# Kernel optimization log

Measured on AMD Instinct MI355X. Metric: run time of the kernel, lower is better.

## Reference

```python
import jax, jax.numpy as jnp
import numpy as np

D_MODEL, D_INNER, D_STATE, DT_RANK, USERS = 2560, 5120, 16, 160, 32

def setup_inputs() -> dict:
    key = jax.random.key(0)
    ks = jax.random.split(key, 16)
    s = lambda k, shp, sc=0.02: (jax.random.normal(k, shp, dtype=jnp.float32) * sc)
    return {
        "x": jax.random.normal(ks[0], (1, 1, USERS, D_MODEL), dtype=jnp.float32),
        "w_in_ssm": s(ks[1], (D_MODEL, D_INNER)),
        "w_in_mlp": s(ks[2], (D_MODEL, D_INNER)),
        "w_out": s(ks[3], (D_INNER, D_MODEL)),
        "conv_w": s(ks[4], (4, D_INNER), 0.5),
        "conv_b": s(ks[5], (D_INNER,), 0.1),
        "conv_state1": jax.random.normal(ks[6], (1, 1, USERS, D_INNER), dtype=jnp.float32),
        "conv_state2": jax.random.normal(ks[7], (1, 1, USERS, D_INNER), dtype=jnp.float32),
        "conv_state3": jax.random.normal(ks[8], (1, 1, USERS, D_INNER), dtype=jnp.float32),
        "x_proj_w": s(ks[9], (D_INNER, DT_RANK + 2 * D_STATE)),
        "dt_proj_w": s(ks[10], (DT_RANK, D_INNER)),
        "dt_proj_b": s(ks[11], (D_INNER,), 0.1),
        "A_log": jax.random.uniform(ks[12], (D_INNER, D_STATE), dtype=jnp.float32),
        "D_param": s(ks[13], (D_INNER,), 1.0),
        "ssm_state": jax.random.normal(ks[14], (USERS, D_INNER, D_STATE), dtype=jnp.float32) * 0.1,
    }

def reference(x, w_in_ssm, w_in_mlp, w_out, conv_w, conv_b,
              conv_state1, conv_state2, conv_state3,
              x_proj_w, dt_proj_w, dt_proj_b, A_log, D_param, ssm_state):
    xb = x.reshape(USERS, D_MODEL)                       # [U, d_model]
    xs = xb @ w_in_ssm                                    # [U, d_inner] (newest conv tap)
    # 4-tap depthwise causal conv via shifted state buffer (unrolled in original)
    taps = (conv_state1.reshape(USERS, D_INNER),
            conv_state2.reshape(USERS, D_INNER),
            conv_state3.reshape(USERS, D_INNER),
            xs)
    c = taps[0] * conv_w[0] + taps[1] * conv_w[1] + taps[2] * conv_w[2] + taps[3] * conv_w[3] + conv_b
    c = jax.nn.silu(c)                                    # [U, d_inner]
    # selective SSM single-step update
    x_dbl = c @ x_proj_w                                  # [U, dt_rank + 2*d_state]
    dt = jax.nn.softplus(x_dbl[:, :DT_RANK] @ dt_proj_w + dt_proj_b)   # [U, d_inner]
    B = x_dbl[:, DT_RANK:DT_RANK + D_STATE]               # [U, d_state]
    C = x_dbl[:, DT_RANK + D_STATE:]                      # [U, d_state]
    A = -jnp.exp(A_log)                                   # [d_inner, d_state]
    dA = jnp.exp(dt[:, :, None] * A[None])                # [U, d_inner, d_state]
    new_state = ssm_state * dA + (dt * c)[:, :, None] * B[:, None, :]
    y = jnp.einsum("uds,us->ud", new_state, C) + D_param * c           # [U, d_inner]
    res = xb @ w_in_mlp                                   # gate branch (no extra silu, per source)
    out = (y * res) @ w_out                               # [U, d_model]
    return out.reshape(1, 1, USERS, D_MODEL)
```

## Files before the change

kernel.cpp:

```cpp
#include <hip/hip_runtime.h>
#include <hip/hip_bf16.h>
#include <cstdint>
#include <cstddef>

#define U   32
#define DM  2560
#define DI  5120
#define DS  16
#define RNK 160
#define XD  192
#define KC1 20
#define KC4 80

typedef __attribute__((ext_vector_type(8)))  short bf16x8;
typedef __attribute__((ext_vector_type(16))) float f32x16;

__device__ __forceinline__ unsigned int pkbf(float a, float b) {
  __hip_bfloat162 h = __float22bfloat162_rn(make_float2(a, b));
  union { __hip_bfloat162 h; unsigned int u; } v; v.h = h; return v.u;
}
__device__ __forceinline__ unsigned short f2bfu(float f) {
  __hip_bfloat16 h = __float2bfloat16(f);
  union { __hip_bfloat16 h; unsigned short u; } v; v.h = h; return v.u;
}
__device__ __forceinline__ float bf2f(unsigned int s) {
  union { float f; unsigned int u; } v; v.u = s << 16; return v.f;
}

__device__ __forceinline__ void gl_lds16(const float* g, float* l) {
  __builtin_amdgcn_global_load_lds(
      (const __attribute__((address_space(1))) unsigned int*)g,
      (__attribute__((address_space(3))) unsigned int*)l,
      16, 0, 0);
}

template<int LDW, int SLAB>
__global__ __launch_bounds__(256, 3) void skinny_dma(
    const float* __restrict__ A, int lda,
    const float* __restrict__ W0, const float* __restrict__ W1,
    unsigned short* __restrict__ part)
{
  constexpr int NS = SLAB / 16;
  __shared__ float        wbuf[2][16][256];
  __shared__ unsigned int albuf[NS][64][4];

  const int tid  = threadIdx.x;
  const int lane = tid & 63, w = tid >> 6;
  const int kcb  = blockIdx.y, z = blockIdx.z;
  const int k0   = kcb * SLAB;
  const float* __restrict__ W = z ? W1 : W0;
  const int col0 = blockIdx.x * 256;

  for (int i = tid; i < U * (SLAB / 2); i += 256) {
    const int u  = i / (SLAB / 2);
    const int kp = i - u * (SLAB / 2);
    const int k  = 2 * kp;
    const float2 v = *(const float2*)&A[(size_t)u * lda + k0 + k];
    albuf[k >> 4][u + U * ((k >> 3) & 1)][(k >> 1) & 3] = pkbf(v.x, v.y);
  }
  __syncthreads();

  const int cl = lane & 31, half = lane >> 5;

  const float* wsrc = W + ((size_t)k0 + w * 4) * LDW + col0 + lane * 4;

#pragma unroll
  for (int i = 0; i < 4; ++i)
    gl_lds16(wsrc + (size_t)i * LDW, &wbuf[0][w * 4 + i][0]);
#pragma unroll
  for (int i = 0; i < 4; ++i)
    gl_lds16(wsrc + (size_t)(16 + i) * LDW, &wbuf[1][w * 4 + i][0]);

  f32x16 acc0{}, acc1{};

#pragma unroll 1
  for (int s = 0; s < NS; ++s) {
    const int buf = s & 1;
    if (s + 1 < NS) { asm volatile("s_waitcnt vmcnt(4)" ::: "memory"); }
    else            { asm volatile("s_waitcnt vmcnt(0)" ::: "memory"); }
    __builtin_amdgcn_s_barrier();

    bf16x8 af = *(const bf16x8*)&albuf[s][lane][0];
#pragma unroll
    for (int f = 0; f < 2; ++f) {
      const int col = w * 64 + f * 32 + cl;
      float r0 = wbuf[buf][half * 8 + 0][col];
      float r1 = wbuf[buf][half * 8 + 1][col];
      float r2 = wbuf[buf][half * 8 + 2][col];
      float r3 = wbuf[buf][half * 8 + 3][col];
      float r4 = wbuf[buf][half * 8 + 4][col];
      float r5 = wbuf[buf][half * 8 + 5][col];
      float r6 = wbuf[buf][half * 8 + 6][col];
      float r7 = wbuf[buf][half * 8 + 7][col];
      union { bf16x8 v; unsigned int d[4]; } bu;
      bu.d[0] = pkbf(r0, r1); bu.d[1] = pkbf(r2, r3);
      bu.d[2] = pkbf(r4, r5); bu.d[3] = pkbf(r6, r7);
      if (f == 0) acc0 = __builtin_amdgcn_mfma_f32_32x32x16_bf16(af, bu.v, acc0, 0, 0, 0);
      else        acc1 = __builtin_amdgcn_mfma_f32_32x32x16_bf16(af, bu.v, acc1, 0, 0, 0);
    }

    asm volatile("" ::: "memory");
    __builtin_amdgcn_s_barrier();
    asm volatile("" ::: "memory");

    if (s + 2 < NS) {
      const float* src = wsrc + (size_t)(s + 2) * 16 * LDW;
#pragma unroll
      for (int i = 0; i < 4; ++i)
        gl_lds16(src + (size_t)i * LDW, &wbuf[buf][w * 4 + i][0]);
    }
  }

  unsigned short* po = part + (size_t)(z * gridDim.y + kcb) * U * LDW + col0;
#pragma unroll
  for (int f = 0; f < 2; ++f) {
    const f32x16& a = f ? acc1 : acc0;
    const int gc = w * 64 + f * 32 + cl;
#pragma unroll
    for (int r = 0; r < 16; ++r) {
      const int m = (r & 3) + 8 * (r >> 2) + 4 * half;
      po[(size_t)m * LDW + gc] = f2bfu(a[r]);
    }
  }
}

__global__ __launch_bounds__(256) void k2a_convsilu(
    const unsigned short* __restrict__ part,
    const float* __restrict__ cs1, const float* __restrict__ cs2,
    const float* __restrict__ cs3,
    const float* __restrict__ cw,  const float* __restrict__ cb,
    float* __restrict__ c_ws, float* __restrict__ res_ws)
{
  const int t = blockIdx.x * 256 + threadIdx.x;
  const int i = 2 * t;
  const int u = i / DI, d = i - u * DI;
  float xs0 = 0.f, xs1 = 0.f, rs0 = 0.f, rs1 = 0.f;
#pragma unroll 4
  for (int kc = 0; kc < KC1; ++kc) {
    unsigned int a = *(const unsigned int*)&part[((size_t)kc * U + u) * DI + d];
    unsigned int b = *(const unsigned int*)&part[((size_t)(KC1 + kc) * U + u) * DI + d];
    xs0 += bf2f(a & 0xffffu); xs1 += bf2f(a >> 16);
    rs0 += bf2f(b & 0xffffu); rs1 += bf2f(b >> 16);
  }
  const float2 s1 = *(const float2*)&cs1[i];
  const float2 s2 = *(const float2*)&cs2[i];
  const float2 s3 = *(const float2*)&cs3[i];
  const float2 w0 = *(const float2*)&cw[d];
  const float2 w1 = *(const float2*)&cw[DI + d];
  const float2 w2 = *(const float2*)&cw[2 * DI + d];
  const float2 w3 = *(const float2*)&cw[3 * DI + d];
  const float2 bb = *(const float2*)&cb[d];
  float c0 = s1.x * w0.x + s2.x * w1.x + s3.x * w2.x + xs0 * w3.x + bb.x;
  float c1 = s1.y * w0.y + s2.y * w1.y + s3.y * w2.y + xs1 * w3.y + bb.y;
  c0 = c0 / (1.f + __expf(-c0));
  c1 = c1 / (1.f + __expf(-c1));
  *(float2*)&c_ws[i]   = make_float2(c0, c1);
  *(float2*)&res_ws[i] = make_float2(rs0, rs1);
}

__global__ __launch_bounds__(256) void k2b_xproj(
    const float* __restrict__ c_ws,
    const float* __restrict__ xpw,
    float* __restrict__ x_dbl)
{
  __shared__ union { float ct[U][80]; float red[4][64][33]; } sh;
  const int k0 = blockIdx.y * 80;

  for (int i4 = threadIdx.x; i4 < U * 20; i4 += 256) {
    int u = i4 / 20, k4 = i4 - u * 20;
    *(float4*)&sh.ct[u][k4 * 4] = *(const float4*)&c_ws[u * DI + k0 + k4 * 4];
  }
  __syncthreads();

  const int c = threadIdx.x & 63, s = threadIdx.x >> 6;
  const int col = blockIdx.x * 64 + c;
  const float* Wp = xpw + (size_t)(k0 + s * 20) * XD + col;

  float acc[U];
#pragma unroll
  for (int u = 0; u < U; ++u) acc[u] = 0.f;

  for (int kk = 0; kk < 20; kk += 4) {
    float w0 = Wp[(size_t)(kk + 0) * XD];
    float w1 = Wp[(size_t)(kk + 1) * XD];
    float w2 = Wp[(size_t)(kk + 2) * XD];
    float w3 = Wp[(size_t)(kk + 3) * XD];
#pragma unroll
    for (int u = 0; u < U; ++u) {
      float4 cv = *(const float4*)&sh.ct[u][s * 20 + kk];
      acc[u] = fmaf(cv.x, w0, acc[u]);
      acc[u] = fmaf(cv.y, w1, acc[u]);
      acc[u] = fmaf(cv.z, w2, acc[u]);
      acc[u] = fmaf(cv.w, w3, acc[u]);
    }
  }

  __syncthreads();
#pragma unroll
  for (int u = 0; u < U; ++u) sh.red[s][c][u] = acc[u];
  __syncthreads();

  for (int p = threadIdx.x; p < 64 * U; p += 256) {
    int cc = p & 63, u = p >> 6;
    float v = sh.red[0][cc][u] + sh.red[1][cc][u] + sh.red[2][cc][u] + sh.red[3][cc][u];
    atomicAdd(&x_dbl[u * XD + blockIdx.x * 64 + cc], v);
  }
}

__global__ __launch_bounds__(256) void k3a_dt(
    const float* __restrict__ x_dbl,
    const float* __restrict__ dpw, const float* __restrict__ dpb,
    float* __restrict__ dt_ws)
{
  __shared__ union { float xt[U][160]; float red[4][64][33]; } sh;

  for (int i4 = threadIdx.x; i4 < U * 40; i4 += 256) {
    int u = i4 / 40, r4 = i4 - u * 40;
    *(float4*)&sh.xt[u][r4 * 4] = *(const float4*)&x_dbl[u * XD + r4 * 4];
  }
  __syncthreads();

  const int c = threadIdx.x & 63, s = threadIdx.x >> 6;
  const int d = blockIdx.x * 64 + c;
  const float* Wp = dpw + (size_t)(s * 40) * DI + d;

  float acc[U];
#pragma unroll
  for (int u = 0; u < U; ++u) acc[u] = 0.f;

  for (int rr = 0; rr < 40; rr += 4) {
    float w0 = Wp[(size_t)(rr + 0) * DI];
    float w1 = Wp[(size_t)(rr + 1) * DI];
    float w2 = Wp[(size_t)(rr + 2) * DI];
    float w3 = Wp[(size_t)(rr + 3) * DI];
#pragma unroll
    for (int u = 0; u < U; ++u) {
      float4 xv = *(const float4*)&sh.xt[u][s * 40 + rr];
      acc[u] = fmaf(xv.x, w0, acc[u]);
      acc[u] = fmaf(xv.y, w1, acc[u]);
      acc[u] = fmaf(xv.z, w2, acc[u]);
      acc[u] = fmaf(xv.w, w3, acc[u]);
    }
  }

  __syncthreads();
#pragma unroll
  for (int u = 0; u < U; ++u) sh.red[s][c][u] = acc[u];
  __syncthreads();

  for (int p = threadIdx.x; p < 64 * U; p += 256) {
    int cc = p & 63, u = p >> 6;
    int dg = blockIdx.x * 64 + cc;
    float pre = sh.red[0][cc][u] + sh.red[1][cc][u] + sh.red[2][cc][u] + sh.red[3][cc][u]
              + dpb[dg];
    float dt = fmaxf(pre, 0.f) + log1pf(expf(-fabsf(pre)));
    dt_ws[u * DI + dg] = dt;
  }
}

__global__ __launch_bounds__(256) void k3b_ssm(
    const float* __restrict__ x_dbl,
    const float* __restrict__ alog, const float* __restrict__ Dp,
    const float* __restrict__ ssm,
    const float* __restrict__ dt_ws,
    const float* __restrict__ c_ws, const float* __restrict__ res_ws,
    float* __restrict__ yr)
{
  const int i = blockIdx.x * 256 + threadIdx.x;
  const int u = i / DI, d = i - u * DI;

  const float dt = dt_ws[i];
  const float cv = c_ws[i];
  const float rv = res_ws[i];
  const float Dv = Dp[d];
  const float dtc = dt * cv;

  float4 B[4], C[4];
#pragma unroll
  for (int q = 0; q < 4; ++q) {
    B[q] = *(const float4*)&x_dbl[u * XD + RNK + q * 4];
    C[q] = *(const float4*)&x_dbl[u * XD + RNK + DS + q * 4];
  }

  const float* st = ssm + ((size_t)u * DI + d) * DS;
  float y = 0.f;
#pragma unroll
  for (int q = 0; q < 4; ++q) {
    float4 al = *(const float4*)&alog[d * DS + q * 4];
    float4 sv = *(const float4*)&st[q * 4];
    y += (sv.x * __expf(dt * -__expf(al.x)) + dtc * B[q].x) * C[q].x;
    y += (sv.y * __expf(dt * -__expf(al.y)) + dtc * B[q].y) * C[q].y;
    y += (sv.z * __expf(dt * -__expf(al.z)) + dtc * B[q].z) * C[q].z;
    y += (sv.w * __expf(dt * -__expf(al.w)) + dtc * B[q].w) * C[q].w;
  }
  y = fmaf(Dv, cv, y);
  yr[i] = y * rv;
}

__global__ __launch_bounds__(256) void k5_reduce(
    const unsigned short* __restrict__ part4,
    float* __restrict__ out)
{
  const int t = blockIdx.x * 256 + threadIdx.x;
  const int i = 2 * t;
  const int u = i / DM, d = i - u * DM;
  float v0 = 0.f, v1 = 0.f;
#pragma unroll 8
  for (int kc = 0; kc < KC4; ++kc) {
    unsigned int a = *(const unsigned int*)&part4[((size_t)kc * U + u) * DM + d];
    v0 += bf2f(a & 0xffffu);
    v1 += bf2f(a >> 16);
  }
  *(float2*)&out[i] = make_float2(v0, v1);
}

extern "C" void kernel_launch(void* const* d_in, const int* in_sizes, int n_in,
                              void* d_out, int out_size, void* d_ws, size_t ws_size,
                              hipStream_t stream)
{
  const float* x    = (const float*)d_in[0];
  const float* wssm = (const float*)d_in[1];
  const float* wmlp = (const float*)d_in[2];
  const float* wout = (const float*)d_in[3];
  const float* cw   = (const float*)d_in[4];
  const float* cb   = (const float*)d_in[5];
  const float* cs1  = (const float*)d_in[6];
  const float* cs2  = (const float*)d_in[7];
  const float* cs3  = (const float*)d_in[8];
  const float* xpw  = (const float*)d_in[9];
  const float* dpw  = (const float*)d_in[10];
  const float* dpb  = (const float*)d_in[11];
  const float* alog = (const float*)d_in[12];
  const float* Dp   = (const float*)d_in[13];
  const float* ssm  = (const float*)d_in[14];
  float* out = (float*)d_out;

  unsigned short* partb = (unsigned short*)d_ws;
  float* c_ws   = (float*)(partb + (size_t)2 * KC1 * U * DI);
  float* res_ws = c_ws   + (size_t)U * DI;
  float* dt_ws  = res_ws + (size_t)U * DI;
  float* yrb    = dt_ws  + (size_t)U * DI;
  float* x_dbl  = yrb    + (size_t)U * DI;

  (void)hipMemsetAsync(x_dbl, 0, (size_t)U * XD * sizeof(float), stream);

  skinny_dma<DI, 128><<<dim3(20, KC1, 2), 256, 0, stream>>>(x, DM, wssm, wmlp, partb);
  k2a_convsilu<<<320, 256, 0, stream>>>(partb, cs1, cs2, cs3, cw, cb, c_ws, res_ws);
  k2b_xproj<<<dim3(3, 64), 256, 0, stream>>>(c_ws, xpw, x_dbl);
  k3a_dt<<<80, 256, 0, stream>>>(x_dbl, dpw, dpb, dt_ws);
  k3b_ssm<<<640, 256, 0, stream>>>(x_dbl, alog, Dp, ssm, dt_ws, c_ws, res_ws, yrb);
  skinny_dma<DM, 64><<<dim3(10, KC4, 1), 256, 0, stream>>>(yrb, DI, wout, wout, partb);
  k5_reduce<<<160, 256, 0, stream>>>(partb, out);
}
```

Before: 86.57 us.

## Fuse middle stages into one cooperative kernel with grid syncs

Merges the conv/silu, x_proj, dt_proj and SSM-update kernels, plus the x_dbl memset, into a single cooperative kernel of 640 blocks that separates the stages with grid.sync(). The aim is to remove several kernel launches and the gaps between them on a latency-bound decode step. In exchange, grid-wide barriers have their own cost, shared memory becomes a union sized to the largest stage, and many blocks sit idle during the narrow x_proj and dt stages. If the cooperative launch fails, it falls back to separate kernels.

```diff
diff --git a/kernel.cpp b/kernel.cpp
--- a/kernel.cpp
+++ b/kernel.cpp
@@ -1,7 +1,10 @@
 #include <hip/hip_runtime.h>
 #include <hip/hip_bf16.h>
+#include <hip/hip_cooperative_groups.h>
 #include <cstdint>
 #include <cstddef>
+
+namespace cg = cooperative_groups;
 
 #define U   32
 #define DM  2560
@@ -61,7 +64,6 @@
   __syncthreads();
 
   const int cl = lane & 31, half = lane >> 5;
-
   const float* wsrc = W + ((size_t)k0 + w * 4) * LDW + col0 + lane * 4;
 
 #pragma unroll
@@ -124,14 +126,14 @@
   }
 }
 
-__global__ __launch_bounds__(256) void k2a_convsilu(
+__device__ __forceinline__ void k2a_body(
+    int t,
     const unsigned short* __restrict__ part,
     const float* __restrict__ cs1, const float* __restrict__ cs2,
     const float* __restrict__ cs3,
     const float* __restrict__ cw,  const float* __restrict__ cb,
     float* __restrict__ c_ws, float* __restrict__ res_ws)
 {
-  const int t = blockIdx.x * 256 + threadIdx.x;
   const int i = 2 * t;
   const int u = i / DI, d = i - u * DI;
   float xs0 = 0.f, xs1 = 0.f, rs0 = 0.f, rs1 = 0.f;
@@ -158,22 +160,22 @@
   *(float2*)&res_ws[i] = make_float2(rs0, rs1);
 }
 
-__global__ __launch_bounds__(256) void k2b_xproj(
-    const float* __restrict__ c_ws,
-    const float* __restrict__ xpw,
+union MidSh { float ct[U][80]; float xt[U][160]; float red[4][64][33]; };
+
+__device__ __forceinline__ void k2b_body(
+    MidSh& sh, int bx, int by, int tid,
+    const float* __restrict__ c_ws, const float* __restrict__ xpw,
     float* __restrict__ x_dbl)
 {
-  __shared__ union { float ct[U][80]; float red[4][64][33]; } sh;
-  const int k0 = blockIdx.y * 80;
-
-  for (int i4 = threadIdx.x; i4 < U * 20; i4 += 256) {
+  const int k0 = by * 80;
+  for (int i4 = tid; i4 < U * 20; i4 += 256) {
     int u = i4 / 20, k4 = i4 - u * 20;
     *(float4*)&sh.ct[u][k4 * 4] = *(const float4*)&c_ws[u * DI + k0 + k4 * 4];
   }
   __syncthreads();
 
-  const int c = threadIdx.x & 63, s = threadIdx.x >> 6;
-  const int col = blockIdx.x * 64 + c;
+  const int c = tid & 63, s = tid >> 6;
+  const int col = bx * 64 + c;
   const float* Wp = xpw + (size_t)(k0 + s * 20) * XD + col;
 
   float acc[U];
@@ -200,28 +202,27 @@
   for (int u = 0; u < U; ++u) sh.red[s][c][u] = acc[u];
   __syncthreads();
 
-  for (int p = threadIdx.x; p < 64 * U; p += 256) {
+  for (int p = tid; p < 64 * U; p += 256) {
     int cc = p & 63, u = p >> 6;
     float v = sh.red[0][cc][u] + sh.red[1][cc][u] + sh.red[2][cc][u] + sh.red[3][cc][u];
-    atomicAdd(&x_dbl[u * XD + blockIdx.x * 64 + cc], v);
-  }
-}
-
-__global__ __launch_bounds__(256) void k3a_dt(
+    atomicAdd(&x_dbl[u * XD + bx * 64 + cc], v);
+  }
+}
+
+__device__ __forceinline__ void k3a_body(
+    MidSh& sh, int bx, int tid,
     const float* __restrict__ x_dbl,
     const float* __restrict__ dpw, const float* __restrict__ dpb,
     float* __restrict__ dt_ws)
 {
-  __shared__ union { float xt[U][160]; float red[4][64][33]; } sh;
-
-  for (int i4 = threadIdx.x; i4 < U * 40; i4 += 256) {
+  for (int i4 = tid; i4 < U * 40; i4 += 256) {
     int u = i4 / 40, r4 = i4 - u * 40;
     *(float4*)&sh.xt[u][r4 * 4] = *(const float4*)&x_dbl[u * XD + r4 * 4];
   }
   __syncthreads();
 
-  const int c = threadIdx.x & 63, s = threadIdx.x >> 6;
-  const int d = blockIdx.x * 64 + c;
+  const int c = tid & 63, s = tid >> 6;
+  const int d = bx * 64 + c;
   const float* Wp = dpw + (size_t)(s * 40) * DI + d;
 
   float acc[U];
@@ -248,9 +249,9 @@
   for (int u = 0; u < U; ++u) sh.red[s][c][u] = acc[u];
   __syncthreads();
 
-  for (int p = threadIdx.x; p < 64 * U; p += 256) {
+  for (int p = tid; p < 64 * U; p += 256) {
     int cc = p & 63, u = p >> 6;
-    int dg = blockIdx.x * 64 + cc;
+    int dg = bx * 64 + cc;
     float pre = sh.red[0][cc][u] + sh.red[1][cc][u] + sh.red[2][cc][u] + sh.red[3][cc][u]
               + dpb[dg];
     float dt = fmaxf(pre, 0.f) + log1pf(expf(-fabsf(pre)));
@@ -258,7 +259,8 @@
   }
 }
 
-__global__ __launch_bounds__(256) void k3b_ssm(
+__device__ __forceinline__ void k3b_body(
+    int i,
     const float* __restrict__ x_dbl,
     const float* __restrict__ alog, const float* __restrict__ Dp,
     const float* __restrict__ ssm,
@@ -266,9 +268,7 @@
     const float* __restrict__ c_ws, const float* __restrict__ res_ws,
     float* __restrict__ yr)
 {
-  const int i = blockIdx.x * 256 + threadIdx.x;
   const int u = i / DI, d = i - u * DI;
-
   const float dt = dt_ws[i];
   const float cv = c_ws[i];
   const float rv = res_ws[i];
@@ -295,6 +295,70 @@
   }
   y = fmaf(Dv, cv, y);
   yr[i] = y * rv;
+}
+
+__global__ __launch_bounds__(256) void fused_mid(
+    const unsigned short* part,
+    const float* cs1, const float* cs2, const float* cs3,
+    const float* cw,  const float* cb,
+    const float* xpw, const float* dpw, const float* dpb,
+    const float* alog, const float* Dp, const float* ssm,
+    float* c_ws, float* res_ws, float* x_dbl, float* dt_ws, float* yr)
+{
+  cg::grid_group grid = cg::this_grid();
+  __shared__ MidSh sh;
+  const int bid = blockIdx.x, tid = threadIdx.x;
+  const int t = bid * 256 + tid;
+
+  if (t < U * DI / 2)
+    k2a_body(t, part, cs1, cs2, cs3, cw, cb, c_ws, res_ws);
+  if (t < U * XD / 2)
+    *(float2*)&x_dbl[2 * t] = make_float2(0.f, 0.f);
+  grid.sync();
+
+  if (bid < 192)
+    k2b_body(sh, bid % 3, bid / 3, tid, c_ws, xpw, x_dbl);
+  grid.sync();
+
+  if (bid < 80)
+    k3a_body(sh, bid, tid, x_dbl, dpw, dpb, dt_ws);
+  grid.sync();
+
+  k3b_body(t, x_dbl, alog, Dp, ssm, dt_ws, c_ws, res_ws, yr);
+}
+
+__global__ __launch_bounds__(256) void k2a_kernel(
+    const unsigned short* __restrict__ part,
+    const float* __restrict__ cs1, const float* __restrict__ cs2,
+    const float* __restrict__ cs3,
+    const float* __restrict__ cw,  const float* __restrict__ cb,
+    float* __restrict__ c_ws, float* __restrict__ res_ws)
+{
+  k2a_body(blockIdx.x * 256 + threadIdx.x, part, cs1, cs2, cs3, cw, cb, c_ws, res_ws);
+}
+__global__ __launch_bounds__(256) void k2b_kernel(
+    const float* __restrict__ c_ws, const float* __restrict__ xpw,
+    float* __restrict__ x_dbl)
+{
+  __shared__ MidSh sh;
+  k2b_body(sh, blockIdx.x, blockIdx.y, threadIdx.x, c_ws, xpw, x_dbl);
+}
+__global__ __launch_bounds__(256) void k3a_kernel(
+    const float* __restrict__ x_dbl,
+    const float* __restrict__ dpw, const float* __restrict__ dpb,
+    float* __restrict__ dt_ws)
+{
+  __shared__ MidSh sh;
+  k3a_body(sh, blockIdx.x, threadIdx.x, x_dbl, dpw, dpb, dt_ws);
+}
+__global__ __launch_bounds__(256) void k3b_kernel(
+    const float* __restrict__ x_dbl,
+    const float* __restrict__ alog, const float* __restrict__ Dp,
+    const float* __restrict__ ssm, const float* __restrict__ dt_ws,
+    const float* __restrict__ c_ws, const float* __restrict__ res_ws,
+    float* __restrict__ yr)
+{
+  k3b_body(blockIdx.x * 256 + threadIdx.x, x_dbl, alog, Dp, ssm, dt_ws, c_ws, res_ws, yr);
 }
 
 __global__ __launch_bounds__(256) void k5_reduce(
@@ -342,13 +406,27 @@
   float* yrb    = dt_ws  + (size_t)U * DI;
   float* x_dbl  = yrb    + (size_t)U * DI;
 
-  (void)hipMemsetAsync(x_dbl, 0, (size_t)U * XD * sizeof(float), stream);
-
   skinny_dma<DI, 128><<<dim3(20, KC1, 2), 256, 0, stream>>>(x, DM, wssm, wmlp, partb);
-  k2a_convsilu<<<320, 256, 0, stream>>>(partb, cs1, cs2, cs3, cw, cb, c_ws, res_ws);
-  k2b_xproj<<<dim3(3, 64), 256, 0, stream>>>(c_ws, xpw, x_dbl);
-  k3a_dt<<<80, 256, 0, stream>>>(x_dbl, dpw, dpb, dt_ws);
-  k3b_ssm<<<640, 256, 0, stream>>>(x_dbl, alog, Dp, ssm, dt_ws, c_ws, res_ws, yrb);
+
+  {
+    const unsigned short* part_c = partb;
+    void* args[] = {
+      (void*)&part_c, (void*)&cs1, (void*)&cs2, (void*)&cs3,
+      (void*)&cw, (void*)&cb, (void*)&xpw, (void*)&dpw, (void*)&dpb,
+      (void*)&alog, (void*)&Dp, (void*)&ssm,
+      (void*)&c_ws, (void*)&res_ws, (void*)&x_dbl, (void*)&dt_ws, (void*)&yrb
+    };
+    hipError_t err = hipLaunchCooperativeKernel(
+        (const void*)fused_mid, dim3(640), dim3(256), args, 0, stream);
+    if (err != hipSuccess) {
+      (void)hipMemsetAsync(x_dbl, 0, (size_t)U * XD * sizeof(float), stream);
+      k2a_kernel<<<320, 256, 0, stream>>>(partb, cs1, cs2, cs3, cw, cb, c_ws, res_ws);
+      k2b_kernel<<<dim3(3, 64), 256, 0, stream>>>(c_ws, xpw, x_dbl);
+      k3a_kernel<<<80, 256, 0, stream>>>(x_dbl, dpw, dpb, dt_ws);
+      k3b_kernel<<<640, 256, 0, stream>>>(x_dbl, alog, Dp, ssm, dt_ws, c_ws, res_ws, yrb);
+    }
+  }
+
   skinny_dma<DM, 64><<<dim3(10, KC4, 1), 256, 0, stream>>>(yrb, DI, wout, wout, partb);
   k5_reduce<<<160, 256, 0, stream>>>(partb, out);
 }
```

Result: slower. 298.0 us (+244.2%).
